# Performance work log

Hardware: AMD Instinct MI355X
Metric: run time of the kernel (lower is better)

## Reference

```python
import jax, jax.numpy as jnp
import numpy as np

B, L, D = 2, 1536, 1024
H, P = 16, 1024
HD = P // H  # 64
K_SIZE = 5
DIFF_STEPS = 3
ALPHA = 0.02
NEG = -1e9
EPS = 1e-9


def setup_inputs() -> dict:
    key = jax.random.key(0)
    ks = jax.random.split(key, 12)
    s = 0.02
    hidden_states = jax.random.normal(ks[0], (B, L, D), dtype=jnp.float32)
    attention_mask = jax.random.randint(ks[1], (B, L), 0, 2, dtype=jnp.int32)
    Wq = jax.random.normal(ks[2], (D, P), dtype=jnp.float32) * s
    bq = jax.random.normal(ks[3], (P,), dtype=jnp.float32) * s
    Wk = jax.random.normal(ks[4], (D, P), dtype=jnp.float32) * s
    bk = jax.random.normal(ks[5], (P,), dtype=jnp.float32) * s
    Wv = jax.random.normal(ks[6], (D, P), dtype=jnp.float32) * s
    bv = jax.random.normal(ks[7], (P,), dtype=jnp.float32) * s
    Wo = jax.random.normal(ks[8], (P, D), dtype=jnp.float32) * s
    bo = jax.random.normal(ks[9], (D,), dtype=jnp.float32) * s
    kernel_w = jax.random.normal(ks[10], (K_SIZE,), dtype=jnp.float32)
    return {"hidden_states": hidden_states, "attention_mask": attention_mask,
            "Wq": Wq, "bq": bq, "Wk": Wk, "bk": bk, "Wv": Wv, "bv": bv,
            "Wo": Wo, "bo": bo, "kernel_w": kernel_w}


def _causal_smooth(p, w):
    # p: (B,H,Lq,Lk); causal cross-correlation matching F.conv1d(pad=k-1)[:Lk]
    k = w.shape[0]
    Lk = p.shape[-1]
    pp = jnp.pad(p, ((0, 0), (0, 0), (0, 0), (k - 1, 0)))
    out = w[0] * pp[..., 0:Lk]
    for j in range(1, k):
        out = out + w[j] * pp[..., j:j + Lk]
    return out


def reference(hidden_states, attention_mask, Wq, bq, Wk, bk, Wv, bv, Wo, bo, kernel_w):
    mask_f = attention_mask.astype(hidden_states.dtype)  # (B,Lk), 1=keep
    additive = (1.0 - mask_f) * NEG                       # (B,Lk)
    key_valid = (attention_mask > 0).astype(hidden_states.dtype)

    Q = (hidden_states @ Wq + bq).reshape(B, L, H, HD)
    Kt = (hidden_states @ Wk + bk).reshape(B, L, H, HD)
    V = (hidden_states @ Wv + bv).reshape(B, L, H, HD)

    scores = jnp.einsum('bqhd,bkhd->bhqk', Q, Kt) / np.sqrt(HD).astype(np.float32)
    scores = scores + additive[:, None, None, :]
    p = jax.nn.softmax(scores, axis=-1)  # (B,H,Lq,Lk)

    w = jax.nn.softmax(kernel_w)  # (k,)
    kv4 = key_valid[:, None, None, :]
    for _ in range(DIFF_STEPS):
        ps = _causal_smooth(p, w)
        ps = ps * kv4
        ps = ps / (jnp.sum(ps, axis=-1, keepdims=True) + EPS)
        p = (1.0 - ALPHA) * p + ALPHA * ps

    attn = jnp.einsum('bhqk,bkhd->bqhd', p, V).reshape(B, L, P)
    return attn @ Wo + bo
```

## Files before the change

kernel.cpp:

```cpp
#include <hip/hip_runtime.h>

#define BB 2
#define LL 1536
#define DD 1024
#define HH 16
#define HDD 64
#define PP 1024

typedef __attribute__((ext_vector_type(8))) __bf16 bf16x8;
typedef __attribute__((ext_vector_type(4))) float f32x4;
typedef __attribute__((ext_vector_type(2))) float f32x2;
typedef _Float16 f16x2 __attribute__((ext_vector_type(2)));
typedef _Float16 f16x8 __attribute__((ext_vector_type(8)));

__device__ __forceinline__ unsigned short f2b(float f) {
  unsigned int x = __builtin_bit_cast(unsigned int, f);
  unsigned int r = (x + 0x7FFFu + ((x >> 16) & 1u)) >> 16;
  return (unsigned short)r;
}
__device__ __forceinline__ bf16x8 ldb8(const unsigned short* p) {
  return __builtin_bit_cast(bf16x8, *(const uint4*)p);
}
__device__ __forceinline__ f16x8 ldh8u(const unsigned int* p) {
  return __builtin_bit_cast(f16x8, *(const uint4*)p);
}
__device__ __forceinline__ unsigned int pkrtz(float lo, float hi) {
  return __builtin_bit_cast(unsigned int, __builtin_amdgcn_cvt_pkrtz(lo, hi));
}
__device__ __forceinline__ float fdot2u(unsigned int a, unsigned int ones,
                                        float c) {
#if __has_builtin(__builtin_amdgcn_fdot2)
  return __builtin_amdgcn_fdot2(__builtin_bit_cast(f16x2, a),
                                __builtin_bit_cast(f16x2, ones), c, false);
#else
  f16x2 x = __builtin_bit_cast(f16x2, a);
  return c + (float)x.x + (float)x.y;
#endif
}
__device__ __forceinline__ void gl_lds16(const unsigned short* g,
                                         unsigned short* l) {
  __builtin_amdgcn_global_load_lds(
      (const __attribute__((address_space(1))) void*)g,
      (__attribute__((address_space(3))) void*)l, 16, 0, 0);
}

__global__ __launch_bounds__(256) void prep(
    const float* __restrict__ hs, unsigned short* __restrict__ hsb,
    const float* __restrict__ Wq, const float* __restrict__ Wk,
    const float* __restrict__ Wv, const float* __restrict__ Wo,
    unsigned short* __restrict__ WT) {
  const int bid = blockIdx.x;
  const int t = threadIdx.x;
  if (bid < 1536) {
    const int idx = bid * 2048 + t * 8;
    float4 a = *(const float4*)(hs + idx);
    float4 b = *(const float4*)(hs + idx + 4);
    uint4 u;
    u.x = (unsigned int)f2b(a.x) | ((unsigned int)f2b(a.y) << 16);
    u.y = (unsigned int)f2b(a.z) | ((unsigned int)f2b(a.w) << 16);
    u.z = (unsigned int)f2b(b.x) | ((unsigned int)f2b(b.y) << 16);
    u.w = (unsigned int)f2b(b.z) | ((unsigned int)f2b(b.w) << 16);
    *(uint4*)(hsb + idx) = u;
  } else {
    __shared__ float tile[64][68];
    const int t2 = bid - 1536;
    const int z = t2 >> 8;
    const int bx = t2 & 15, by = (t2 >> 4) & 15;
    const float* W = (z == 0) ? Wq : (z == 1) ? Wk : (z == 2) ? Wv : Wo;
    unsigned short* O = WT + (size_t)z * 1024 * 1024;
    const int r0 = by * 64;
    const int c0 = bx * 64;
#pragma unroll
    for (int i = 0; i < 4; ++i) {
      const int row = (t >> 4) + i * 16;
      const int col = (t & 15) * 4;
      *(float4*)&tile[row][col] =
          *(const float4*)&W[(size_t)(r0 + row) * 1024 + c0 + col];
    }
    __syncthreads();
#pragma unroll
    for (int i = 0; i < 4; ++i) {
      const int n = (t >> 4) + i * 16;
      const int k4 = (t & 15) * 4;
      uint2 u;
      u.x = (unsigned int)f2b(tile[k4 + 0][n]) |
            ((unsigned int)f2b(tile[k4 + 1][n]) << 16);
      u.y = (unsigned int)f2b(tile[k4 + 2][n]) |
            ((unsigned int)f2b(tile[k4 + 3][n]) << 16);
      *(uint2*)&O[(size_t)(c0 + n) * 1024 + r0 + k4] = u;
    }
  }
}

template <int MODE>
__device__ __forceinline__ void gemm_mfma_body(
    const unsigned short* __restrict__ A, const unsigned short* __restrict__ Bt,
    const float* __restrict__ bias, void* __restrict__ Cout) {
  __shared__ unsigned short As[128 * 32];
  __shared__ unsigned short Bs[128 * 32];
  const int t = threadIdx.x;
  const int lane = t & 63;
  const int w = t >> 6;
  const int quad = lane >> 4;
  const int lc = lane & 15;
  const int m0 = blockIdx.y * 128, n0 = blockIdx.x * 128;

  const int sr = lane >> 2;
  const int sk = (lane & 3) * 8;
  const unsigned short* ga0 = A + (size_t)(m0 + w * 32 + sr) * 1024 + sk;
  const unsigned short* ga1 = ga0 + 16 * 1024;
  const unsigned short* gb0 = Bt + (size_t)(n0 + w * 32 + sr) * 1024 + sk;
  const unsigned short* gb1 = gb0 + 16 * 1024;
  unsigned short* la0 = As + w * 1024;
  unsigned short* la1 = As + w * 1024 + 512;
  unsigned short* lb0 = Bs + w * 1024;
  unsigned short* lb1 = Bs + w * 1024 + 512;

  const int mrow0 = (w >> 1) * 64, ncol0 = (w & 1) * 64;

  f32x4 acc[4][4];
#pragma unroll
  for (int i = 0; i < 4; ++i)
#pragma unroll
    for (int j = 0; j < 4; ++j) acc[i][j] = (f32x4){0.f, 0.f, 0.f, 0.f};

  for (int k0 = 0; k0 < 1024; k0 += 32) {
    __syncthreads();
    gl_lds16(ga0 + k0, la0);
    gl_lds16(ga1 + k0, la1);
    gl_lds16(gb0 + k0, lb0);
    gl_lds16(gb1 + k0, lb1);
    __syncthreads();
    bf16x8 af[4], bfr[4];
#pragma unroll
    for (int i = 0; i < 4; ++i)
      af[i] = ldb8(&As[(mrow0 + i * 16 + lc) * 32 + quad * 8]);
#pragma unroll
    for (int j = 0; j < 4; ++j)
      bfr[j] = ldb8(&Bs[(ncol0 + j * 16 + lc) * 32 + quad * 8]);
#pragma unroll
    for (int i = 0; i < 4; ++i)
#pragma unroll
      for (int j = 0; j < 4; ++j)
        acc[i][j] = __builtin_amdgcn_mfma_f32_16x16x32_bf16(af[i], bfr[j],
                                                            acc[i][j], 0, 0, 0);
  }

#pragma unroll
  for (int i = 0; i < 4; ++i) {
    const int row0 = m0 + mrow0 + i * 16 + quad * 4;
#pragma unroll
    for (int jj = 0; jj < 4; ++jj) {
      const int col = n0 + ncol0 + jj * 16 + lc;
      const float bz = bias[col];
      float o[4];
#pragma unroll
      for (int r = 0; r < 4; ++r) o[r] = acc[i][jj][r] + bz;
      if constexpr (MODE == 0) {
        const int bb = row0 / LL;
        const int ql = row0 - bb * LL;
        const int qt = ql >> 4;
        const int m = ql & 15;
        const int hh = col >> 6;
        const int hd = col & 63;
        const int f = hd >> 5;
        const int qk = (hd >> 3) & 3;
        const int j = hd & 7;
        unsigned short* QF = (unsigned short*)Cout;
        const size_t base = (((size_t)(bb * HH + hh) * 96 + qt) * 2 + f) * 512 +
                            (qk * 16 + m) * 8 + j;
#pragma unroll
        for (int r = 0; r < 4; ++r) QF[base + r * 8] = f2b(o[r] * 0.125f);
      } else if constexpr (MODE == 1) {
        const int bb = row0 / LL;
        const int kl = row0 - bb * LL;
        const int ktl = kl >> 4;
        const int m = kl & 15;
        const int hh = col >> 6;
        const int hd = col & 63;
        const int f = hd >> 5;
        const int qk = (hd >> 3) & 3;
        const int j = hd & 7;
        unsigned short* KF = (unsigned short*)Cout;
        const size_t base =
            (((size_t)(bb * HH + hh) * 96 + ktl) * 2 + f) * 512 +
            (qk * 16 + m) * 8 + j;
#pragma unroll
        for (int r = 0; r < 4; ++r) KF[base + r * 8] = f2b(o[r]);
      } else if constexpr (MODE == 2) {
        const int bb = row0 / LL;
        const int kl = row0 - bb * LL;
        const int hh = col >> 6;
        const int hd = col & 63;
        const int hg = hd >> 4;
        const int lcv = hd & 15;
        const int tile = (kl >> 5);
        const int qv = (kl >> 3) & 3;
        const int j0 = kl & 7;
        unsigned short* VF = (unsigned short*)Cout;
        const size_t base = (((size_t)(bb * HH + hh) * 4 + hg) * 48 + tile) * 512 +
                            (qv * 16 + lcv) * 8 + j0;
        uint2 u;
        u.x = pkrtz(o[0], o[1]);
        u.y = pkrtz(o[2], o[3]);
        *(uint2*)&VF[base] = u;
      } else {
#pragma unroll
        for (int r = 0; r < 4; ++r)
          ((float*)Cout)[(size_t)(row0 + r) * 1024 + col] = o[r];
      }
    }
  }
}

__global__ __launch_bounds__(256) void qkv_gemm(
    const unsigned short* __restrict__ hsb,
    const unsigned short* __restrict__ WT, const float* __restrict__ bq,
    const float* __restrict__ bk, const float* __restrict__ bv,
    unsigned short* __restrict__ QF, unsigned short* __restrict__ KF,
    unsigned short* __restrict__ VF) {
  if (blockIdx.z == 0) {
    gemm_mfma_body<0>(hsb, WT, bq, QF);
  } else if (blockIdx.z == 1) {
    gemm_mfma_body<1>(hsb, WT + 1024 * 1024, bk, KF);
  } else {
    gemm_mfma_body<2>(hsb, WT + 2 * 1024 * 1024, bv, VF);
  }
}

__global__ __launch_bounds__(256) void out_gemm(
    const unsigned short* __restrict__ ctxb,
    const unsigned short* __restrict__ WoT, const float* __restrict__ bo,
    float* __restrict__ out) {
  gemm_mfma_body<3>(ctxb, WoT, bo, out);
}

__global__ __launch_bounds__(1024)
    __attribute__((amdgpu_waves_per_eu(8))) void attn_kernel(
        const unsigned short* __restrict__ QF,
        const unsigned short* __restrict__ KF,
        const unsigned short* __restrict__ VF, const int* __restrict__ mask,
        const float* __restrict__ kernel_w, unsigned short* __restrict__ ctxb) {
  __shared__ __align__(16) unsigned int P2u[97 * 192];
  __shared__ unsigned int kvb[48];
  __shared__ float red_a[16][16];
  __shared__ float red_b[16][16];
  __shared__ float wext[48];

  const int t = threadIdx.x;
  const int lane = t & 63;
  const int w = t >> 6;
  const int quad = lane >> 4;
  const int lc = lane & 15;
  const int b = blockIdx.z, h = blockIdx.y;
  const int q0 = blockIdx.x * 16;

  {
    unsigned long long bal = __ballot(mask[b * LL + t] > 0);
    if (lane == 0) {
      kvb[2 * w] = (unsigned int)bal;
      kvb[2 * w + 1] = (unsigned int)(bal >> 32);
    }
  }
  if (w < 8) {
    unsigned long long bal = __ballot(mask[b * LL + 1024 + t] > 0);
    if (lane == 0) {
      kvb[32 + 2 * w] = (unsigned int)bal;
      kvb[33 + 2 * w] = (unsigned int)(bal >> 32);
    }
  }
  if (t < 192) P2u[t] = 0;
  {
    float k0 = kernel_w[0], k1 = kernel_w[1], k2 = kernel_w[2],
          k3 = kernel_w[3], k4 = kernel_w[4];
    float km = fmaxf(fmaxf(fmaxf(k0, k1), fmaxf(k2, k3)), k4);
    float e0 = __expf(k0 - km), e1 = __expf(k1 - km), e2 = __expf(k2 - km),
          e3 = __expf(k3 - km), e4 = __expf(k4 - km);
    float es = e0 + e1 + e2 + e3 + e4;
    if (t < 48) {
      float v = 0.f;
      if (t == 16) v = e4 / es;
      if (t == 17) v = e3 / es;
      if (t == 18) v = e2 / es;
      if (t == 19) v = e1 / es;
      if (t == 20) v = e0 / es;
      wext[t] = v;
    }
  }
  __syncthreads();

  f16x8 afb;
  {
    const int kb = lc + 32 - quad * 8;
    uint4 uu;
    uu.x = pkrtz(wext[kb], wext[kb - 1]);
    uu.y = pkrtz(wext[kb - 2], wext[kb - 3]);
    uu.z = pkrtz(wext[kb - 4], wext[kb - 5]);
    uu.w = pkrtz(wext[kb - 6], wext[kb - 7]);
    afb = __builtin_bit_cast(f16x8, uu);
  }

  unsigned int* const pwb = &P2u[((6 * w + 1) * 16 + lc) * 12 + 2 * quad];
  unsigned int mA = 0u;
  {
    const unsigned short* qfb =
        QF + (((size_t)(b * HH + h) * 96 + (q0 >> 4)) * 2) * 512 + lane * 8;
    const bf16x8 qb0 = ldb8(qfb);
    const bf16x8 qb1 = ldb8(qfb + 512);
    const unsigned short* kfb =
        KF + (((size_t)(b * HH + h) * 96 + 6 * w) * 2) * 512 + lane * 8;
    float s = 0.f;
#pragma unroll
    for (int j = 0; j < 6; ++j) {
      bf16x8 ka0 = ldb8(kfb + j * 1024);
      bf16x8 ka1 = ldb8(kfb + j * 1024 + 512);
      f32x4 acc = {0.f, 0.f, 0.f, 0.f};
      acc = __builtin_amdgcn_mfma_f32_16x16x32_bf16(ka0, qb0, acc, 0, 0, 0);
      acc = __builtin_amdgcn_mfma_f32_16x16x32_bf16(ka1, qb1, acc, 0, 0, 0);
      const int kb16 = 16 * j + 4 * quad;
      const unsigned int w4 = (kvb[3 * w + (kb16 >> 5)] >> (kb16 & 31)) & 0xFu;
      mA |= w4 << (4 * j);
      float e0 = (w4 & 1u) ? __expf(acc[0]) : 0.f;
      float e1 = (w4 & 2u) ? __expf(acc[1]) : 0.f;
      float e2 = (w4 & 4u) ? __expf(acc[2]) : 0.f;
      float e3 = (w4 & 8u) ? __expf(acc[3]) : 0.f;
      uint2 u;
      u.x = pkrtz(e0, e1);
      u.y = pkrtz(e2, e3);
      *(uint2*)(pwb + j * 192) = u;
      s += (e0 + e1) + (e2 + e3);
    }
    s += __shfl_xor(s, 16, 64);
    s += __shfl_xor(s, 32, 64);
    if (lane < 16) red_a[w][lane] = s;
  }
  __syncthreads();

  const unsigned int ones2 = 0x3C003C00u;
  const unsigned int* const prb =
      &P2u[((6 * w + (quad >> 1)) * 16 + lc) * 12 + (quad & 1) * 4];
  float inv = 0.f;
#pragma unroll
  for (int step = 0; step < 3; ++step) {
    unsigned int s_pk[12];
    float sum = 0.f;
#pragma unroll
    for (int j = 0; j < 6; ++j) {
      f16x8 bfr = ldh8u(prb + j * 192);
      f32x4 z = {0.f, 0.f, 0.f, 0.f};
      f32x4 ps = __builtin_amdgcn_mfma_f32_16x16x32_f16(afb, bfr, z, 0, 0, 0);
      const unsigned int w4 = (mA >> (4 * j)) & 0xFu;
      float p0 = (w4 & 1u) ? ps[0] : 0.f;
      float p1 = (w4 & 2u) ? ps[1] : 0.f;
      float p2 = (w4 & 4u) ? ps[2] : 0.f;
      float p3 = (w4 & 8u) ? ps[3] : 0.f;
      s_pk[2 * j] = pkrtz(p0, p1);
      s_pk[2 * j + 1] = pkrtz(p2, p3);
      sum = fdot2u(s_pk[2 * j], ones2, sum);
      sum = fdot2u(s_pk[2 * j + 1], ones2, sum);
    }
    sum += __shfl_xor(sum, 16, 64);
    sum += __shfl_xor(sum, 32, 64);
    if (step == 0) {
      float tot0 = 0.f;
#pragma unroll
      for (int ww = 0; ww < 16; ++ww) tot0 += red_a[ww][lc];
      inv = 1.f / tot0;
    }
    if (lane < 16) {
      if (step & 1)
        red_a[w][lane] = sum;
      else
        red_b[w][lane] = sum;
    }
    __syncthreads();
    float tot = 0.f;
#pragma unroll
    for (int ww = 0; ww < 16; ++ww)
      tot += (step & 1) ? red_a[ww][lc] : red_b[ww][lc];
    f16x2 cmul, cinv, cps;
    if (step == 0) {
      const float sps = tot * inv;
      const float pinv = 0.02f / (sps + 1e-9f);
      const _Float16 hc = (_Float16)(0.98f * inv);
      const _Float16 hi = (_Float16)inv;
      const _Float16 hp = (_Float16)pinv;
      cmul = (f16x2){hc, hc};
      cinv = (f16x2){hi, hi};
      cps = (f16x2){hp, hp};
    } else {
      const float pinv = 0.02f / (tot + 1e-9f);
      const _Float16 hp = (_Float16)pinv;
      cmul = (f16x2){(_Float16)0.98f, (_Float16)0.98f};
      cinv = (f16x2){(_Float16)1.f, (_Float16)1.f};
      cps = (f16x2){hp, hp};
    }
#pragma unroll
    for (int j = 0; j < 6; ++j) {
      uint2 po = *(const uint2*)(pwb + j * 192);
      f16x2 p0h = __builtin_bit_cast(f16x2, po.x);
      f16x2 p1h = __builtin_bit_cast(f16x2, po.y);
      f16x2 s0h = __builtin_bit_cast(f16x2, s_pk[2 * j]);
      f16x2 s1h = __builtin_bit_cast(f16x2, s_pk[2 * j + 1]);
      p0h = p0h * cmul + (s0h * cinv) * cps;
      p1h = p1h * cmul + (s1h * cinv) * cps;
      uint2 nu;
      nu.x = __builtin_bit_cast(unsigned int, p0h);
      nu.y = __builtin_bit_cast(unsigned int, p1h);
      *(uint2*)(pwb + j * 192) = nu;
    }
    __syncthreads();
  }

  const int cg = w & 3;
  const int kt = w >> 2;
  const int cidx = cg * 16 + lc;
  const int li = (cg * 4 + quad) * 16 + lc;
  const unsigned short* vfb =
      VF + ((((size_t)(b * HH + h) * 4 + cg) * 48 + 12 * kt) * 512) + lane * 8;
  const unsigned int* const pvb =
      &P2u[((24 * kt + 1 + (quad >> 1)) * 16 + lc) * 12 + (quad & 1) * 4];
  f32x4 oacc = {0.f, 0.f, 0.f, 0.f};
#pragma unroll
  for (int g = 0; g < 6; ++g) {
#pragma unroll
    for (int c = 0; c < 2; ++c) {
      f16x8 pa = ldh8u(pvb + (4 * g + 2 * c) * 192);
      f16x8 vf =
          __builtin_bit_cast(f16x8, *(const uint4*)(vfb + (2 * g + c) * 512));
      oacc = __builtin_amdgcn_mfma_f32_16x16x32_f16(pa, vf, oacc, 0, 0, 0);
    }
  }
  if (kt > 0) {
    float* sp = (float*)&P2u[((kt - 1) * 256 + li) * 12 + 8];
    *(float4*)sp = make_float4(oacc[0], oacc[1], oacc[2], oacc[3]);
  }
  __syncthreads();
  if (kt == 0) {
    float o[4] = {oacc[0], oacc[1], oacc[2], oacc[3]};
#pragma unroll
    for (int p = 0; p < 3; ++p) {
      const float4 prr = *(const float4*)&P2u[(p * 256 + li) * 12 + 8];
      o[0] += prr.x;
      o[1] += prr.y;
      o[2] += prr.z;
      o[3] += prr.w;
    }
#pragma unroll
    for (int r = 0; r < 4; ++r)
      ctxb[((size_t)(b * LL + q0 + quad * 4 + r)) * PP + h * HDD + cidx] =
          f2b(o[r]);
  }
}

extern "C" void kernel_launch(void* const* d_in, const int* in_sizes, int n_in,
                              void* d_out, int out_size, void* d_ws,
                              size_t ws_size, hipStream_t stream) {
  const float* hs = (const float*)d_in[0];
  const int* mask = (const int*)d_in[1];
  const float* Wq = (const float*)d_in[2];
  const float* bq = (const float*)d_in[3];
  const float* Wk = (const float*)d_in[4];
  const float* bk = (const float*)d_in[5];
  const float* Wv = (const float*)d_in[6];
  const float* bv = (const float*)d_in[7];
  const float* Wo = (const float*)d_in[8];
  const float* bo = (const float*)d_in[9];
  const float* kw = (const float*)d_in[10];

  const size_t NBLP = (size_t)BB * LL * PP;
  unsigned short* QF = (unsigned short*)d_ws;
  unsigned short* KF = QF + NBLP;
  unsigned short* VF = KF + NBLP;
  unsigned short* ctxb = VF + NBLP;
  unsigned short* hsb = ctxb + NBLP;
  unsigned short* WT = hsb + NBLP;

  dim3 blk(256);
  prep<<<dim3(2560), blk, 0, stream>>>(hs, hsb, Wq, Wk, Wv, Wo, WT);
  qkv_gemm<<<dim3(8, 24, 3), blk, 0, stream>>>(hsb, WT, bq, bk, bv, QF, KF, VF);
  attn_kernel<<<dim3(96, 16, 2), dim3(1024), 0, stream>>>(QF, KF, VF, mask, kw,
                                                          ctxb);
  out_gemm<<<dim3(8, 24, 1), blk, 0, stream>>>(ctxb, WT + 3 * 1024 * 1024, bo,
                                               (float*)d_out);
}
```

Before: 236.4 us.

## Double-buffer GEMM LDS tiles and swizzle block-to-tile mapping

```diff
diff --git a/kernel.cpp b/kernel.cpp
--- a/kernel.cpp
+++ b/kernel.cpp
@@ -95,15 +95,15 @@
 template <int MODE>
 __device__ __forceinline__ void gemm_mfma_body(
     const unsigned short* __restrict__ A, const unsigned short* __restrict__ Bt,
-    const float* __restrict__ bias, void* __restrict__ Cout) {
-  __shared__ unsigned short As[128 * 32];
-  __shared__ unsigned short Bs[128 * 32];
+    const float* __restrict__ bias, void* __restrict__ Cout, const int m0,
+    const int n0) {
+  __shared__ unsigned short As[2 * 128 * 32];
+  __shared__ unsigned short Bs[2 * 128 * 32];
   const int t = threadIdx.x;
   const int lane = t & 63;
   const int w = t >> 6;
   const int quad = lane >> 4;
   const int lc = lane & 15;
-  const int m0 = blockIdx.y * 128, n0 = blockIdx.x * 128;
 
   const int sr = lane >> 2;
   const int sk = (lane & 3) * 8;
@@ -111,10 +111,8 @@
   const unsigned short* ga1 = ga0 + 16 * 1024;
   const unsigned short* gb0 = Bt + (size_t)(n0 + w * 32 + sr) * 1024 + sk;
   const unsigned short* gb1 = gb0 + 16 * 1024;
-  unsigned short* la0 = As + w * 1024;
-  unsigned short* la1 = As + w * 1024 + 512;
-  unsigned short* lb0 = Bs + w * 1024;
-  unsigned short* lb1 = Bs + w * 1024 + 512;
+  unsigned short* const laA = As + w * 1024;
+  unsigned short* const laB = Bs + w * 1024;
 
   const int mrow0 = (w >> 1) * 64, ncol0 = (w & 1) * 64;
 
@@ -124,26 +122,41 @@
 #pragma unroll
     for (int j = 0; j < 4; ++j) acc[i][j] = (f32x4){0.f, 0.f, 0.f, 0.f};
 
-  for (int k0 = 0; k0 < 1024; k0 += 32) {
-    __syncthreads();
-    gl_lds16(ga0 + k0, la0);
-    gl_lds16(ga1 + k0, la1);
-    gl_lds16(gb0 + k0, lb0);
-    gl_lds16(gb1 + k0, lb1);
-    __syncthreads();
+  auto stage = [&](int buf, int k0) {
+    unsigned short* a = laA + buf * 4096;
+    unsigned short* bp = laB + buf * 4096;
+    gl_lds16(ga0 + k0, a);
+    gl_lds16(ga1 + k0, a + 512);
+    gl_lds16(gb0 + k0, bp);
+    gl_lds16(gb1 + k0, bp + 512);
+  };
+  auto compute = [&](int buf) {
+    const unsigned short* Ab = As + buf * 4096;
+    const unsigned short* Bb = Bs + buf * 4096;
     bf16x8 af[4], bfr[4];
 #pragma unroll
     for (int i = 0; i < 4; ++i)
-      af[i] = ldb8(&As[(mrow0 + i * 16 + lc) * 32 + quad * 8]);
+      af[i] = ldb8(&Ab[(mrow0 + i * 16 + lc) * 32 + quad * 8]);
 #pragma unroll
     for (int j = 0; j < 4; ++j)
-      bfr[j] = ldb8(&Bs[(ncol0 + j * 16 + lc) * 32 + quad * 8]);
+      bfr[j] = ldb8(&Bb[(ncol0 + j * 16 + lc) * 32 + quad * 8]);
 #pragma unroll
     for (int i = 0; i < 4; ++i)
 #pragma unroll
       for (int j = 0; j < 4; ++j)
         acc[i][j] = __builtin_amdgcn_mfma_f32_16x16x32_bf16(af[i], bfr[j],
                                                             acc[i][j], 0, 0, 0);
+  };
+
+  stage(0, 0);
+  __syncthreads();
+  for (int it = 0; it < 32; it += 2) {
+    stage(1, (it + 1) * 32);
+    compute(0);
+    __syncthreads();
+    if (it + 2 < 32) stage(0, (it + 2) * 32);
+    compute(1);
+    __syncthreads();
   }
 
 #pragma unroll
@@ -213,18 +226,27 @@
   }
 }
 
+__device__ __forceinline__ void swz192(int& m0, int& n0) {
+  const int lin = blockIdx.y * 8 + blockIdx.x;
+  const int swz = (lin & 7) * 24 + (lin >> 3);
+  m0 = (swz >> 3) * 128;
+  n0 = (swz & 7) * 128;
+}
+
 __global__ __launch_bounds__(256) void qkv_gemm(
     const unsigned short* __restrict__ hsb,
     const unsigned short* __restrict__ WT, const float* __restrict__ bq,
     const float* __restrict__ bk, const float* __restrict__ bv,
     unsigned short* __restrict__ QF, unsigned short* __restrict__ KF,
     unsigned short* __restrict__ VF) {
+  int m0, n0;
+  swz192(m0, n0);
   if (blockIdx.z == 0) {
-    gemm_mfma_body<0>(hsb, WT, bq, QF);
+    gemm_mfma_body<0>(hsb, WT, bq, QF, m0, n0);
   } else if (blockIdx.z == 1) {
-    gemm_mfma_body<1>(hsb, WT + 1024 * 1024, bk, KF);
+    gemm_mfma_body<1>(hsb, WT + 1024 * 1024, bk, KF, m0, n0);
   } else {
-    gemm_mfma_body<2>(hsb, WT + 2 * 1024 * 1024, bv, VF);
+    gemm_mfma_body<2>(hsb, WT + 2 * 1024 * 1024, bv, VF, m0, n0);
   }
 }
 
@@ -232,7 +254,9 @@
     const unsigned short* __restrict__ ctxb,
     const unsigned short* __restrict__ WoT, const float* __restrict__ bo,
     float* __restrict__ out) {
-  gemm_mfma_body<3>(ctxb, WoT, bo, out);
+  int m0, n0;
+  swz192(m0, n0);
+  gemm_mfma_body<3>(ctxb, WoT, bo, out, m0, n0);
 }
 
 __global__ __launch_bounds__(1024)
```

Measured after the change: 267.0 us. 12.9% more time.
